# Kernel tuning notes

Hardware: AMD Instinct MI355X
Metric: run time of the kernel (lower is better)

Reference implementation:

```python
import jax, jax.numpy as jnp
import numpy as np

D_MODEL = 1024
NUM_HEADS = 16
HEAD_DIM = D_MODEL // NUM_HEADS
B, S = 4, 2048


def setup_inputs() -> dict:
    key = jax.random.key(0)
    ks = jax.random.split(key, 11)
    scale = 1.0 / np.sqrt(D_MODEL)
    return {
        "query": jax.random.normal(ks[0], (B, S, D_MODEL), dtype=jnp.float32),
        "key": jax.random.normal(ks[1], (B, S, D_MODEL), dtype=jnp.float32),
        "value": jax.random.normal(ks[2], (B, S, D_MODEL), dtype=jnp.float32),
        "Wq": jax.random.normal(ks[3], (D_MODEL, D_MODEL), dtype=jnp.float32) * scale,
        "bq": jnp.zeros((D_MODEL,), dtype=jnp.float32),
        "Wk": jax.random.normal(ks[4], (D_MODEL, D_MODEL), dtype=jnp.float32) * scale,
        "bk": jnp.zeros((D_MODEL,), dtype=jnp.float32),
        "Wv": jax.random.normal(ks[5], (D_MODEL, D_MODEL), dtype=jnp.float32) * scale,
        "bv": jnp.zeros((D_MODEL,), dtype=jnp.float32),
        "Wo": jax.random.normal(ks[6], (D_MODEL, D_MODEL), dtype=jnp.float32) * scale,
        "bo": jnp.zeros((D_MODEL,), dtype=jnp.float32),
    }


def reference(query, key, value, Wq, bq, Wk, bk, Wv, bv, Wo, bo):
    b = query.shape[0]
    # QKV projections, split into heads: [B, H, S, hd]
    Q = (query @ Wq + bq).reshape(b, -1, NUM_HEADS, HEAD_DIM).transpose(0, 2, 1, 3)
    K = (key @ Wk + bk).reshape(b, -1, NUM_HEADS, HEAD_DIM).transpose(0, 2, 1, 3)
    V = (value @ Wv + bv).reshape(b, -1, NUM_HEADS, HEAD_DIM).transpose(0, 2, 1, 3)
    # scaled dot-product attention, full [B, H, S, S] scores (as in original)
    scores = jnp.einsum("bhqd,bhkd->bhqk", Q, K) / jnp.sqrt(
        jnp.asarray(HEAD_DIM, dtype=jnp.float32))
    attn = jax.nn.softmax(scores, axis=-1)
    out = jnp.einsum("bhqk,bhkd->bhqd", attn, V)
    out = out.transpose(0, 2, 1, 3).reshape(b, -1, D_MODEL)
    return out @ Wo + bo
```

## Files before the change

kernel.cpp:

```cpp
#include <hip/hip_runtime.h>
#include <hip/hip_bf16.h>

typedef _Float16 f16;
typedef _Float16 f16x8 __attribute__((ext_vector_type(8)));
typedef _Float16 f16x4 __attribute__((ext_vector_type(4)));
typedef __fp16 h16x2 __attribute__((ext_vector_type(2)));
typedef float f32x4 __attribute__((ext_vector_type(4)));

#define D_MODEL 1024
#define NHEAD 16
#define HD 64
#define BATCH 4
#define SEQ 2048
#define TOK (BATCH * SEQ)

__device__ __forceinline__ void gload_lds16(const void* g, void* l) {
  __builtin_amdgcn_global_load_lds(
      (const __attribute__((address_space(1))) unsigned int*)g,
      (__attribute__((address_space(3))) unsigned int*)l, 16, 0, 0);
}

__device__ __forceinline__ f16x8 fragF16_64(const char* rowptr, int g, int c) {
  union { uint4 u; f16x8 v; } r;
  r.u = *reinterpret_cast<const uint4*>(rowptr + ((g * 16) ^ ((c & 3) << 4)));
  return r.v;
}
__device__ __forceinline__ f16x8 fragF32_128(const char* rowptr, int g, int c) {
  const int s = (c & 7) << 4;
  union { uint4 u; float f[4]; } a, b;
  a.u = *reinterpret_cast<const uint4*>(rowptr + ((g * 32) ^ s));
  b.u = *reinterpret_cast<const uint4*>(rowptr + ((g * 32 + 16) ^ s));
  f16x8 r;
  r[0] = (f16)a.f[0]; r[1] = (f16)a.f[1]; r[2] = (f16)a.f[2]; r[3] = (f16)a.f[3];
  r[4] = (f16)b.f[0]; r[5] = (f16)b.f[1]; r[6] = (f16)b.f[2]; r[7] = (f16)b.f[3];
  return r;
}
__device__ __forceinline__ f16x8 lds_frag(const char* rowptr, int cb0, int s) {
  const uint2 a = *reinterpret_cast<const uint2*>(rowptr + (cb0 ^ s));
  const uint2 b = *reinterpret_cast<const uint2*>(rowptr + ((cb0 + 32) ^ s));
  union { unsigned int u[4]; f16x8 v; } r;
  r.u[0] = a.x; r.u[1] = a.y; r.u[2] = b.x; r.u[3] = b.y;
  return r.v;
}

__global__ __launch_bounds__(256) void transpose_cvt4_k(
    const float* __restrict__ w0, const float* __restrict__ w1,
    const float* __restrict__ w2, const float* __restrict__ w3,
    f16* __restrict__ t0, f16* __restrict__ t1, f16* __restrict__ t2,
    f16* __restrict__ t3) {
  __shared__ float tile[32][33];
  const float* W = blockIdx.z == 0 ? w0 : blockIdx.z == 1 ? w1 : blockIdx.z == 2 ? w2 : w3;
  f16* Wt = blockIdx.z == 0 ? t0 : blockIdx.z == 1 ? t1 : blockIdx.z == 2 ? t2 : t3;
  int n0 = blockIdx.x * 32, k0 = blockIdx.y * 32;
  int tx = threadIdx.x & 31, ty = threadIdx.x >> 5;
#pragma unroll
  for (int i = 0; i < 32; i += 8)
    tile[ty + i][tx] = W[(size_t)(k0 + ty + i) * D_MODEL + n0 + tx];
  __syncthreads();
#pragma unroll
  for (int i = 0; i < 32; i += 8)
    Wt[(size_t)(n0 + ty + i) * D_MODEL + k0 + tx] = (f16)tile[tx][ty + i];
}

template <bool A_F32, bool B_F32, bool OUT_F32, bool BIAS_ROW>
__global__ __launch_bounds__(256) void gemm_k(
    const void* __restrict__ Ap, const void* __restrict__ Bp,
    const float* __restrict__ bias, void* __restrict__ Cout,
    int M, int N, int K, float scale) {
  constexpr int ABUF = A_F32 ? 16384 : 8192;
  constexpr int BBUF = B_F32 ? 16384 : 8192;
  constexpr int BUF = ABUF + BBUF;
  constexpr int NA = A_F32 ? 4 : 2;
  constexpr int NB = B_F32 ? 4 : 2;
  __shared__ char smem[2 * BUF];
  const int tid = threadIdx.x;
  const int lane = tid & 63, wid = tid >> 6;
  const int g = lane >> 4, c = lane & 15;
  const int wm = wid >> 1, wn = wid & 1;
  const size_t brow = (size_t)blockIdx.y * 128, bcol = (size_t)blockIdx.x * 128;

  f32x4 acc[4][4];
#pragma unroll
  for (int i = 0; i < 4; ++i)
#pragma unroll
    for (int j = 0; j < 4; ++j) acc[i][j] = (f32x4){0.f, 0.f, 0.f, 0.f};

  const char* ga[NA];
  const char* gb[NB];
#pragma unroll
  for (int j = 0; j < NA; ++j) {
    int ch = wid * NA + j;
    if constexpr (A_F32) {
      int row = ch * 8 + (lane >> 3);
      ga[j] = (const char*)Ap + ((size_t)(brow + row) * K) * 4 +
              (((lane & 7) * 16) ^ ((row & 7) << 4));
    } else {
      int row = ch * 16 + (lane >> 2);
      ga[j] = (const char*)Ap + ((size_t)(brow + row) * K) * 2 +
              (((lane & 3) * 16) ^ ((row & 3) << 4));
    }
  }
#pragma unroll
  for (int j = 0; j < NB; ++j) {
    int ch = wid * NB + j;
    if constexpr (B_F32) {
      int row = ch * 8 + (lane >> 3);
      gb[j] = (const char*)Bp + ((size_t)(bcol + row) * K) * 4 +
              (((lane & 7) * 16) ^ ((row & 7) << 4));
    } else {
      int row = ch * 16 + (lane >> 2);
      gb[j] = (const char*)Bp + ((size_t)(bcol + row) * K) * 2 +
              (((lane & 3) * 16) ^ ((row & 3) << 4));
    }
  }
  auto stage = [&](char* buf) {
#pragma unroll
    for (int j = 0; j < NA; ++j) {
      gload_lds16(ga[j], buf + (wid * NA + j) * 1024);
      ga[j] += A_F32 ? 128 : 64;
    }
#pragma unroll
    for (int j = 0; j < NB; ++j) {
      gload_lds16(gb[j], buf + ABUF + (wid * NB + j) * 1024);
      gb[j] += B_F32 ? 128 : 64;
    }
  };

  stage(smem);
  const int nt = K / 32;
  for (int t = 0; t < nt; ++t) {
    char* cur = smem + (size_t)(t & 1) * BUF;
    char* nxt = smem + (size_t)((t + 1) & 1) * BUF;
    asm volatile("s_waitcnt vmcnt(0)" ::: "memory");
    __syncthreads();
    if (t + 1 < nt) stage(nxt);

    f16x8 Af[4], Bf[4];
#pragma unroll
    for (int fm = 0; fm < 4; ++fm) {
      int row = wm * 64 + fm * 16 + c;
      if constexpr (A_F32) Af[fm] = fragF32_128(cur + row * 128, g, c);
      else Af[fm] = fragF16_64(cur + row * 64, g, c);
    }
#pragma unroll
    for (int fn = 0; fn < 4; ++fn) {
      int row = wn * 64 + fn * 16 + c;
      if constexpr (B_F32) Bf[fn] = fragF32_128(cur + ABUF + row * 128, g, c);
      else Bf[fn] = fragF16_64(cur + ABUF + row * 64, g, c);
    }
#pragma unroll
    for (int fm = 0; fm < 4; ++fm)
#pragma unroll
      for (int fn = 0; fn < 4; ++fn)
        acc[fm][fn] = __builtin_amdgcn_mfma_f32_16x16x32_f16(Af[fm], Bf[fn],
                                                             acc[fm][fn], 0, 0, 0);
  }

#pragma unroll
  for (int fn = 0; fn < 4; ++fn) {
    size_t col = bcol + wn * 64 + fn * 16 + c;
    float cbias = BIAS_ROW ? 0.f : bias[col];
#pragma unroll
    for (int fm = 0; fm < 4; ++fm) {
#pragma unroll
      for (int r = 0; r < 4; ++r) {
        size_t row = brow + wm * 64 + fm * 16 + g * 4 + r;
        float v = (acc[fm][fn][r] + (BIAS_ROW ? bias[row] : cbias)) * scale;
        if (OUT_F32)
          ((float*)Cout)[row * (size_t)N + col] = v;
        else
          ((f16*)Cout)[row * (size_t)N + col] = (f16)v;
      }
    }
  }
}

__global__ __launch_bounds__(512) void attn_k(const f16* __restrict__ Q,
                                              const f16* __restrict__ Kp,
                                              const f16* __restrict__ Vt,
                                              f16* __restrict__ AO) {
  __shared__ char smem[32768];
  const int tid = threadIdx.x, lane = tid & 63, wid = tid >> 6;
  const int g = lane >> 4, c = lane & 15;
  const int qt = blockIdx.x;
  const int b = blockIdx.y >> 4, h = blockIdx.y & 15;
  const size_t qrow0 = (size_t)b * SEQ + (size_t)qt * 256;
  const int sr = lane >> 3;
  const int sc = (lane & 7) * 16;
  const float NEG_M = -8.65617025f;

#pragma unroll
  for (int j = 0; j < 4; ++j) {
    int ch = wid * 4 + j;
    int row = ch * 8 + sr;
    const char* gq = (const char*)Q + ((qrow0 + row) * D_MODEL + h * HD) * 2 +
                     (sc ^ (sr << 4));
    gload_lds16(gq, smem + ch * 1024);
  }
  asm volatile("s_waitcnt vmcnt(0)" ::: "memory");
  __syncthreads();

  f16x8 Qf[2][2];
#pragma unroll
  for (int fq = 0; fq < 2; ++fq) {
    int row = wid * 32 + fq * 16 + c;
#pragma unroll
    for (int kk = 0; kk < 2; ++kk) {
      union { uint4 u; f16x8 v; } r;
      r.u = *reinterpret_cast<const uint4*>(
          smem + row * 128 + ((kk * 64 + g * 16) ^ ((c & 7) << 4)));
      Qf[fq][kk] = r.v;
    }
  }
  __syncthreads();

  const char* gk;
  const char* gv;
  {
    int row = wid * 8 + sr;
    gk = (const char*)Kp + (((size_t)b * SEQ + row) * D_MODEL + h * HD) * 2 +
         (sc ^ (sr << 4));
    gv = (const char*)Vt + ((size_t)(h * HD + row) * TOK + (size_t)b * SEQ) * 2 +
         (sc ^ (sr << 4));
  }
  gload_lds16(gk, smem + wid * 1024);
  gload_lds16(gv, smem + 8192 + wid * 1024);
  gk += (size_t)64 * D_MODEL * 2;
  gv += 64 * 2;

  f16x8 ones_f;
#pragma unroll
  for (int j = 0; j < 8; ++j) ones_f[j] = (c == 0) ? (f16)1.0f : (f16)0.0f;

  f32x4 o[4][2];
#pragma unroll
  for (int i = 0; i < 4; ++i)
#pragma unroll
    for (int j = 0; j < 2; ++j) o[i][j] = (f32x4){0.f, 0.f, 0.f, 0.f};
  f32x4 o_l[2] = {(f32x4){0.f, 0.f, 0.f, 0.f}, (f32x4){0.f, 0.f, 0.f, 0.f}};

  for (int t = 0; t < SEQ / 64; ++t) {
    char* cur = smem + (size_t)(t & 1) * 16384;
    char* nxt = smem + (size_t)((t + 1) & 1) * 16384;
    asm volatile("s_waitcnt vmcnt(0)" ::: "memory");
    __syncthreads();
    if (t + 1 < SEQ / 64) {
      gload_lds16(gk, nxt + wid * 1024);
      gload_lds16(gv, nxt + 8192 + wid * 1024);
      gk += (size_t)64 * D_MODEL * 2;
      gv += 64 * 2;
    }
    const char* Ks = cur;
    const char* Vs = cur + 8192;

    f32x4 st[4][2];
#pragma unroll
    for (int i = 0; i < 4; ++i)
#pragma unroll
      for (int j = 0; j < 2; ++j)
        st[i][j] = (f32x4){NEG_M, NEG_M, NEG_M, NEG_M};
#pragma unroll
    for (int kk = 0; kk < 2; ++kk) {
      f16x8 Kf[4];
#pragma unroll
      for (int km = 0; km < 4; ++km) {
        int row = km * 16 + c;
        union { uint4 u; f16x8 v; } r;
        r.u = *reinterpret_cast<const uint4*>(
            Ks + row * 128 + ((kk * 64 + g * 16) ^ ((c & 7) << 4)));
        Kf[km] = r.v;
      }
      __builtin_amdgcn_s_setprio(1);
#pragma unroll
      for (int km = 0; km < 4; ++km)
#pragma unroll
        for (int fq = 0; fq < 2; ++fq)
          st[km][fq] = __builtin_amdgcn_mfma_f32_16x16x32_f16(Kf[km], Qf[fq][kk],
                                                              st[km][fq], 0, 0, 0);
      __builtin_amdgcn_s_setprio(0);
    }

    f16x8 pb[2][2];
#pragma unroll
    for (int fq = 0; fq < 2; ++fq) {
#pragma unroll
      for (int km = 0; km < 4; ++km)
#pragma unroll
        for (int r = 0; r < 4; ++r)
          st[km][fq][r] = __builtin_amdgcn_exp2f(st[km][fq][r]);
#pragma unroll
      for (int k2 = 0; k2 < 2; ++k2) {
        union { h16x2 h2[4]; f16x8 v; } u;
        u.h2[0] = __builtin_amdgcn_cvt_pkrtz(st[2 * k2][fq][0], st[2 * k2][fq][1]);
        u.h2[1] = __builtin_amdgcn_cvt_pkrtz(st[2 * k2][fq][2], st[2 * k2][fq][3]);
        u.h2[2] = __builtin_amdgcn_cvt_pkrtz(st[2 * k2 + 1][fq][0], st[2 * k2 + 1][fq][1]);
        u.h2[3] = __builtin_amdgcn_cvt_pkrtz(st[2 * k2 + 1][fq][2], st[2 * k2 + 1][fq][3]);
        pb[k2][fq] = u.v;
      }
    }

#pragma unroll
    for (int k2 = 0; k2 < 2; ++k2) {
      f16x8 Vf[4];
#pragma unroll
      for (int fhd = 0; fhd < 4; ++fhd) {
        int row = fhd * 16 + c;
        Vf[fhd] = lds_frag(Vs + row * 128, k2 * 64 + g * 8, (row & 7) << 4);
      }
      __builtin_amdgcn_s_setprio(1);
#pragma unroll
      for (int fhd = 0; fhd < 4; ++fhd)
#pragma unroll
        for (int fq = 0; fq < 2; ++fq)
          o[fhd][fq] = __builtin_amdgcn_mfma_f32_16x16x32_f16(Vf[fhd], pb[k2][fq],
                                                              o[fhd][fq], 0, 0, 0);
#pragma unroll
      for (int fq = 0; fq < 2; ++fq)
        o_l[fq] = __builtin_amdgcn_mfma_f32_16x16x32_f16(ones_f, pb[k2][fq],
                                                         o_l[fq], 0, 0, 0);
      __builtin_amdgcn_s_setprio(0);
    }
  }

#pragma unroll
  for (int fq = 0; fq < 2; ++fq) {
    float L = __shfl(o_l[fq][0], c);
    float rl = 1.0f / L;
    size_t token = qrow0 + wid * 32 + fq * 16 + c;
#pragma unroll
    for (int fhd = 0; fhd < 4; ++fhd) {
      f16x4 vv;
#pragma unroll
      for (int r = 0; r < 4; ++r) vv[r] = (f16)(o[fhd][fq][r] * rl);
      *reinterpret_cast<f16x4*>(AO + token * D_MODEL + h * HD + fhd * 16 + g * 4) = vv;
    }
  }
}

extern "C" void kernel_launch(void* const* d_in, const int* in_sizes, int n_in,
                              void* d_out, int out_size, void* d_ws, size_t ws_size,
                              hipStream_t stream) {
  const float* q32 = (const float*)d_in[0];
  const float* k32 = (const float*)d_in[1];
  const float* v32 = (const float*)d_in[2];
  const float* Wq = (const float*)d_in[3];
  const float* bq = (const float*)d_in[4];
  const float* Wk = (const float*)d_in[5];
  const float* bk = (const float*)d_in[6];
  const float* Wv = (const float*)d_in[7];
  const float* bv = (const float*)d_in[8];
  const float* Wo = (const float*)d_in[9];
  const float* bo = (const float*)d_in[10];

  const size_t TOKD = (size_t)TOK * D_MODEL;
  const size_t WD = (size_t)D_MODEL * D_MODEL;
  f16* Qp = (f16*)d_ws;
  f16* Kp = Qp + TOKD;
  f16* Vt = Kp + TOKD;
  f16* AO = Vt + TOKD;
  f16* Wqt = AO + TOKD;
  f16* Wkt = Wqt + WD;
  f16* Wvt = Wkt + WD;
  f16* Wot = Wvt + WD;

  dim3 tg(32, 32, 4);
  transpose_cvt4_k<<<tg, 256, 0, stream>>>(Wq, Wk, Wv, Wo, Wqt, Wkt, Wvt, Wot);

  dim3 gq(D_MODEL / 128, TOK / 128);
  gemm_k<true, false, false, false><<<gq, 256, 0, stream>>>(
      q32, Wqt, bq, Qp, TOK, D_MODEL, D_MODEL, 0.18033688f);
  gemm_k<true, false, false, false><<<gq, 256, 0, stream>>>(
      k32, Wkt, bk, Kp, TOK, D_MODEL, D_MODEL, 1.0f);
  dim3 gv(TOK / 128, D_MODEL / 128);
  gemm_k<false, true, false, true><<<gv, 256, 0, stream>>>(
      Wvt, v32, bv, Vt, D_MODEL, TOK, D_MODEL, 1.0f);

  dim3 ga(SEQ / 256, BATCH * NHEAD);
  attn_k<<<ga, 512, 0, stream>>>(Qp, Kp, Vt, AO);

  gemm_k<false, false, true, false><<<gq, 256, 0, stream>>>(
      AO, Wot, bo, (float*)d_out, TOK, D_MODEL, D_MODEL, 1.0f);
}
```

Before: 233.5 us.

## Software-pipeline attention loop: overlap QK of next tile with PV of previous

Restructures the attention inner loop so the QK^T MFMAs for tile t are interleaved with the PV MFMAs for tile t-1, with a prologue and epilogue. K stays double-buffered while V becomes triple-buffered in LDS (40 KB) to keep the lagged V tile valid. It also swaps the grid order so blocks sharing a batch and head are spread differently across the GPU, and adds an occupancy hint to launch_bounds. Extra LDS and live registers (st and pb both live across the loop) could reduce occupancy or cause spills.

Result: slower. 281.5 us (+20.6%).

```diff
diff --git a/kernel.cpp b/kernel.cpp
--- a/kernel.cpp
+++ b/kernel.cpp
@@ -175,19 +175,20 @@
   }
 }
 
-__global__ __launch_bounds__(512) void attn_k(const f16* __restrict__ Q,
-                                              const f16* __restrict__ Kp,
-                                              const f16* __restrict__ Vt,
-                                              f16* __restrict__ AO) {
-  __shared__ char smem[32768];
+__global__ __launch_bounds__(512, 4) void attn_k(const f16* __restrict__ Q,
+                                                 const f16* __restrict__ Kp,
+                                                 const f16* __restrict__ Vt,
+                                                 f16* __restrict__ AO) {
+  __shared__ char smem[40960];
   const int tid = threadIdx.x, lane = tid & 63, wid = tid >> 6;
   const int g = lane >> 4, c = lane & 15;
-  const int qt = blockIdx.x;
-  const int b = blockIdx.y >> 4, h = blockIdx.y & 15;
+  const int b = blockIdx.x >> 4, h = blockIdx.x & 15;
+  const int qt = blockIdx.y;
   const size_t qrow0 = (size_t)b * SEQ + (size_t)qt * 256;
   const int sr = lane >> 3;
   const int sc = (lane & 7) * 16;
   const float NEG_M = -8.65617025f;
+  constexpr int NT = SEQ / 64;
 
 #pragma unroll
   for (int j = 0; j < 4; ++j) {
@@ -224,9 +225,15 @@
          (sc ^ (sr << 4));
   }
   gload_lds16(gk, smem + wid * 1024);
-  gload_lds16(gv, smem + 8192 + wid * 1024);
+  gload_lds16(gv, smem + 16384 + wid * 1024);
   gk += (size_t)64 * D_MODEL * 2;
-  gv += 64 * 2;
+  gv += 128;
+  asm volatile("s_waitcnt vmcnt(0)" ::: "memory");
+  __syncthreads();
+  gload_lds16(gk, smem + 8192 + wid * 1024);
+  gload_lds16(gv, smem + 16384 + 8192 + wid * 1024);
+  gk += (size_t)64 * D_MODEL * 2;
+  gv += 128;
 
   f16x8 ones_f;
 #pragma unroll
@@ -239,48 +246,49 @@
     for (int j = 0; j < 2; ++j) o[i][j] = (f32x4){0.f, 0.f, 0.f, 0.f};
   f32x4 o_l[2] = {(f32x4){0.f, 0.f, 0.f, 0.f}, (f32x4){0.f, 0.f, 0.f, 0.f}};
 
-  for (int t = 0; t < SEQ / 64; ++t) {
-    char* cur = smem + (size_t)(t & 1) * 16384;
-    char* nxt = smem + (size_t)((t + 1) & 1) * 16384;
-    asm volatile("s_waitcnt vmcnt(0)" ::: "memory");
-    __syncthreads();
-    if (t + 1 < SEQ / 64) {
-      gload_lds16(gk, nxt + wid * 1024);
-      gload_lds16(gv, nxt + 8192 + wid * 1024);
-      gk += (size_t)64 * D_MODEL * 2;
-      gv += 64 * 2;
-    }
-    const char* Ks = cur;
-    const char* Vs = cur + 8192;
-
-    f32x4 st[4][2];
-#pragma unroll
-    for (int i = 0; i < 4; ++i)
-#pragma unroll
-      for (int j = 0; j < 2; ++j)
-        st[i][j] = (f32x4){NEG_M, NEG_M, NEG_M, NEG_M};
-#pragma unroll
-    for (int kk = 0; kk < 2; ++kk) {
-      f16x8 Kf[4];
-#pragma unroll
-      for (int km = 0; km < 4; ++km) {
-        int row = km * 16 + c;
-        union { uint4 u; f16x8 v; } r;
-        r.u = *reinterpret_cast<const uint4*>(
-            Ks + row * 128 + ((kk * 64 + g * 16) ^ ((c & 7) << 4)));
-        Kf[km] = r.v;
-      }
-      __builtin_amdgcn_s_setprio(1);
-#pragma unroll
-      for (int km = 0; km < 4; ++km)
-#pragma unroll
-        for (int fq = 0; fq < 2; ++fq)
-          st[km][fq] = __builtin_amdgcn_mfma_f32_16x16x32_f16(Kf[km], Qf[fq][kk],
-                                                              st[km][fq], 0, 0, 0);
-      __builtin_amdgcn_s_setprio(0);
-    }
-
-    f16x8 pb[2][2];
+  f32x4 st[4][2];
+  f16x8 pb[2][2];
+
+  auto qk_cluster = [&](const char* Ks, int kk) {
+    f16x8 Kf[4];
+#pragma unroll
+    for (int km = 0; km < 4; ++km) {
+      int row = km * 16 + c;
+      union { uint4 u; f16x8 v; } r;
+      r.u = *reinterpret_cast<const uint4*>(
+          Ks + row * 128 + ((kk * 64 + g * 16) ^ ((c & 7) << 4)));
+      Kf[km] = r.v;
+    }
+    __builtin_amdgcn_s_setprio(1);
+#pragma unroll
+    for (int km = 0; km < 4; ++km)
+#pragma unroll
+      for (int fq = 0; fq < 2; ++fq)
+        st[km][fq] = __builtin_amdgcn_mfma_f32_16x16x32_f16(Kf[km], Qf[fq][kk],
+                                                            st[km][fq], 0, 0, 0);
+    __builtin_amdgcn_s_setprio(0);
+  };
+  auto pv_cluster = [&](const char* Vs, int k2) {
+    f16x8 Vf[4];
+#pragma unroll
+    for (int fhd = 0; fhd < 4; ++fhd) {
+      int row = fhd * 16 + c;
+      Vf[fhd] = lds_frag(Vs + row * 128, k2 * 64 + g * 8, (row & 7) << 4);
+    }
+    __builtin_amdgcn_s_setprio(1);
+#pragma unroll
+    for (int fhd = 0; fhd < 4; ++fhd)
+#pragma unroll
+      for (int fq = 0; fq < 2; ++fq)
+        o[fhd][fq] = __builtin_amdgcn_mfma_f32_16x16x32_f16(Vf[fhd], pb[k2][fq],
+                                                            o[fhd][fq], 0, 0, 0);
+#pragma unroll
+    for (int fq = 0; fq < 2; ++fq)
+      o_l[fq] = __builtin_amdgcn_mfma_f32_16x16x32_f16(ones_f, pb[k2][fq],
+                                                       o_l[fq], 0, 0, 0);
+    __builtin_amdgcn_s_setprio(0);
+  };
+  auto softmax_pack = [&]() {
 #pragma unroll
     for (int fq = 0; fq < 2; ++fq) {
 #pragma unroll
@@ -298,28 +306,43 @@
         pb[k2][fq] = u.v;
       }
     }
-
-#pragma unroll
-    for (int k2 = 0; k2 < 2; ++k2) {
-      f16x8 Vf[4];
-#pragma unroll
-      for (int fhd = 0; fhd < 4; ++fhd) {
-        int row = fhd * 16 + c;
-        Vf[fhd] = lds_frag(Vs + row * 128, k2 * 64 + g * 8, (row & 7) << 4);
-      }
-      __builtin_amdgcn_s_setprio(1);
-#pragma unroll
-      for (int fhd = 0; fhd < 4; ++fhd)
-#pragma unroll
-        for (int fq = 0; fq < 2; ++fq)
-          o[fhd][fq] = __builtin_amdgcn_mfma_f32_16x16x32_f16(Vf[fhd], pb[k2][fq],
-                                                              o[fhd][fq], 0, 0, 0);
-#pragma unroll
-      for (int fq = 0; fq < 2; ++fq)
-        o_l[fq] = __builtin_amdgcn_mfma_f32_16x16x32_f16(ones_f, pb[k2][fq],
-                                                         o_l[fq], 0, 0, 0);
-      __builtin_amdgcn_s_setprio(0);
-    }
+  };
+
+#pragma unroll
+  for (int i = 0; i < 4; ++i)
+#pragma unroll
+    for (int j = 0; j < 2; ++j) st[i][j] = (f32x4){NEG_M, NEG_M, NEG_M, NEG_M};
+  qk_cluster(smem, 0);
+  qk_cluster(smem, 1);
+  softmax_pack();
+
+  for (int t = 1; t < NT; ++t) {
+    asm volatile("s_waitcnt vmcnt(0)" ::: "memory");
+    __syncthreads();
+    if (t + 1 < NT) {
+      gload_lds16(gk, smem + ((t + 1) & 1) * 8192 + wid * 1024);
+      gload_lds16(gv, smem + 16384 + ((t + 1) % 3) * 8192 + wid * 1024);
+      gk += (size_t)64 * D_MODEL * 2;
+      gv += 128;
+    }
+    const char* Ks = smem + (t & 1) * 8192;
+    const char* Vs = smem + 16384 + ((t - 1) % 3) * 8192;
+
+#pragma unroll
+    for (int i = 0; i < 4; ++i)
+#pragma unroll
+      for (int j = 0; j < 2; ++j) st[i][j] = (f32x4){NEG_M, NEG_M, NEG_M, NEG_M};
+    qk_cluster(Ks, 0);
+    pv_cluster(Vs, 0);
+    qk_cluster(Ks, 1);
+    pv_cluster(Vs, 1);
+    softmax_pack();
+  }
+
+  {
+    const char* Vs = smem + 16384 + ((NT - 1) % 3) * 8192;
+    pv_cluster(Vs, 0);
+    pv_cluster(Vs, 1);
   }
 
 #pragma unroll
@@ -375,7 +398,7 @@
   gemm_k<false, true, false, true><<<gv, 256, 0, stream>>>(
       Wvt, v32, bv, Vt, D_MODEL, TOK, D_MODEL, 1.0f);
 
-  dim3 ga(SEQ / 256, BATCH * NHEAD);
+  dim3 ga(BATCH * NHEAD, SEQ / 256);
   attn_k<<<ga, 512, 0, stream>>>(Qp, Kp, Vt, AO);
 
   gemm_k<false, false, true, false><<<gq, 256, 0, stream>>>(
```
